# Kernel tuning notes

Hardware: AMD Instinct MI355X
Metric: run time of the kernel (lower is better)

## Reference

```python
import jax, jax.numpy as jnp
import numpy as np
import math

WS = 7          # window size (hardcoded in RelativeSinusoidalEmbeddings)
NUM_HEADS = 12

def _rel_embeddings(ws=WS):
    # Faithful replica of RelativeSinusoidalEmbeddings.__init__
    C = 2 * ws - 1
    B = np.zeros((C, C), dtype=np.float32)
    positions = np.arange(C, dtype=np.float32)[:, None]
    divisor = np.exp(np.arange(0, C, 2, dtype=np.float32) * (-math.log(10000.0) / C))
    angles = positions * divisor
    B[:, 0::2] = np.sin(angles)
    B[:, 1::2] = np.cos(angles[:, :-1])
    x = np.arange(1.0, ws + 1.0, 1.0 / ws)                 # length ws*ws
    xi = (x[None, :] - x[:, None]).astype(np.int32)        # trunc toward zero, like torch .int()
    y = np.concatenate([np.arange(1, ws + 1)] * ws)
    yi = y[None, :] - y[:, None]
    return jnp.asarray(B[xi, yi])                           # [ws^2, ws^2]

def _shift_masks(ws=WS):
    n = ws * ws
    s = ws * (ws // 2)
    row = np.zeros((n, n), dtype=np.float32)
    row[-s:, : n - s] = -np.inf
    row[: n - s, -s:] = -np.inf
    # rearrange '(r w1) (c w2) -> (w1 r) (w2 c)'
    col = row.reshape(ws, ws, ws, ws).transpose(1, 0, 3, 2).reshape(n, n)
    return jnp.asarray(row), jnp.asarray(col)

_EMB = _rel_embeddings()
_ROW_MASK, _COL_MASK = _shift_masks()

def setup_inputs() -> dict:
    key = jax.random.key(0)
    k1, k2, k3 = jax.random.split(key, 3)
    B, H, W, D = 16, 56, 56, 384
    return {
        "x": jax.random.normal(k1, (B, H, W, D), dtype=jnp.float32),
        "w_qkv": jax.random.normal(k2, (D, 3 * D), dtype=jnp.float32) * 0.02,
        "b_qkv": jnp.zeros((3 * D,), dtype=jnp.float32),
        "w_out": jax.random.normal(k3, (D, D), dtype=jnp.float32) * 0.02,
        "b_out": jnp.zeros((D,), dtype=jnp.float32),
    }

def reference(x, w_qkv, b_qkv, w_out, b_out):
    B, Hh, Ww, d = x.shape
    ws, nh = WS, NUM_HEADS
    E = d // nh
    h, w = Hh // ws, Ww // ws
    # qkv projection, split last dim as (c, K=3) per rearrange 'b h w (c K)'
    qkv = (x @ w_qkv + b_qkv).reshape(B, Hh, Ww, d, 3)
    # mask is active since Hh != 7; shift is -ws//2 == -4 (faithful to source)
    qkv = jnp.roll(qkv, (-ws // 2, -ws // 2), axis=(1, 2))
    # 'b (h m1) (w m2) (H E) K -> b H h w (m1 m2) E K'
    qkv = qkv.reshape(B, h, ws, w, ws, nh, E, 3)
    qkv = qkv.transpose(0, 5, 1, 3, 2, 4, 6, 7).reshape(B, nh, h, w, ws * ws, E, 3)
    Q, K, V = qkv[..., 0], qkv[..., 1], qkv[..., 2]
    scores = jnp.einsum('bnhwqe,bnhwke->bnhwqk', Q, K) / math.sqrt(d / nh)
    scores = scores + _EMB
    scores = scores.at[:, :, -1, :].add(_ROW_MASK)   # last row of window grid
    scores = scores.at[:, :, :, -1].add(_COL_MASK)   # last col of window grid
    att = jax.nn.softmax(scores, axis=-1) @ V         # [B, nh, h, w, ws^2, E]
    # 'b H h w (m1 m2) E -> b (h m1) (w m2) (H E)'
    out = att.reshape(B, nh, h, w, ws, ws, E)
    out = out.transpose(0, 2, 4, 3, 5, 1, 6).reshape(B, Hh, Ww, d)
    out = jnp.roll(out, (ws // 2, ws // 2), axis=(1, 2))  # unshift by +3 (as in source)
    return out @ w_out + b_out
```

## Files before the change

### kernel.cpp

```cpp
#include <hip/hip_runtime.h>
#include <math.h>

#define DIM   384
#define NQKV  1152
#define IMG   56
#define ROWS_PER_B (IMG*IMG)

typedef unsigned short u16;
typedef unsigned int u32;
typedef __attribute__((ext_vector_type(2))) unsigned int u32x2;
typedef __attribute__((ext_vector_type(4))) float f32x4;
typedef __attribute__((ext_vector_type(8))) short s16x8;

__device__ __forceinline__ u16 f2b(float f) {
    unsigned u = __float_as_uint(f);
    return (u16)((u + 0x7fffu + ((u >> 16) & 1u)) >> 16);
}

__device__ __forceinline__ void gl2lds16(const void* g, void* l) {
    __builtin_amdgcn_global_load_lds(
        (const __attribute__((address_space(1))) void*)g,
        (__attribute__((address_space(3))) void*)l, 16, 0, 0);
}

__global__ __launch_bounds__(256) void emb4_init_kernel(float* __restrict__ emb4) {
    int idx = blockIdx.x * 256 + threadIdx.x;
    if (idx >= 64 * 64) return;
    int q = idx >> 6, k = idx & 63;

    bool pad = (q >= 49) || (k >= 49);
    float base = 0.f;
    if (!pad) {
        const double step  = 1.0 / 7.0;
        const double delta = __dsub_rn(__dadd_rn(1.0, step), 1.0);
        double xk = __dadd_rn(1.0, __dmul_rn((double)k, delta));
        double xq = __dadd_rn(1.0, __dmul_rn((double)q, delta));
        int xi = (int)__dsub_rn(xk, xq);
        int yi = (k % 7) - (q % 7);
        int r = xi % 13; if (r < 0) r += 13;
        int c = yi % 13; if (c < 0) c += 13;
        const float scl = (float)(-0.7084877209212449);
        if ((c & 1) == 0) base = sinf((float)r * expf((float)c * scl));
        else              base = cosf((float)r * expf((float)(c - 1) * scl));
    }
    bool rmask = !pad && ((q >= 28) != (k >= 28));
    bool cmask = !pad && ((q % 7 >= 4) != (k % 7 >= 4));
    #pragma unroll
    for (int v = 0; v < 4; ++v) {
        float val = base;
        if (pad || ((v & 1) && rmask) || ((v & 2) && cmask)) val = -INFINITY;
        emb4[v * 4096 + idx] = val;
    }
}

__global__ __launch_bounds__(256) void cvt_f32_bf16(
    const float* __restrict__ in, u16* __restrict__ out, int n4) {
    int i = blockIdx.x * 256 + threadIdx.x;
    if (i >= n4) return;
    float4 v = ((const float4*)in)[i];
    ushort4 o;
    o.x = f2b(v.x); o.y = f2b(v.y); o.z = f2b(v.z); o.w = f2b(v.w);
    ((ushort4*)out)[i] = o;
}

__global__ __launch_bounds__(256) void cvt_transpose_bf16(
    const float* __restrict__ w, u16* __restrict__ wt, int R, int C) {
    int i = blockIdx.x * 256 + threadIdx.x;
    if (i >= R * C) return;
    int r = i / C, c = i % C;
    wt[(size_t)c * R + r] = f2b(w[i]);
}

__global__ __launch_bounds__(256) void cvt_transpose_qkv(
    const float* __restrict__ w, u16* __restrict__ wt) {
    int i = blockIdx.x * 256 + threadIdx.x;
    if (i >= 384 * 1152) return;
    int k = i / 1152, col = i % 1152;
    int ch = col / 3, comp = col % 3;
    int np = comp * 384 + ch;
    wt[(size_t)np * 384 + k] = f2b(w[i]);
}

__global__ __launch_bounds__(256) void bias_perm_kernel(
    const float* __restrict__ b, float* __restrict__ bp) {
    int n = blockIdx.x * 256 + threadIdx.x;
    if (n >= 1152) return;
    int comp = n / 384, ch = n % 384;
    bp[n] = b[ch * 3 + comp];
}

template <int MODE>
__global__ __launch_bounds__(512, 6) void mfma_gemm(
    const u16* __restrict__ A, const u16* __restrict__ Bt,
    const float* __restrict__ bias,
    u16* __restrict__ outb, float* __restrict__ outf,
    int N, int K)
{
    __shared__ __align__(16) u16 As[2][8192];
    __shared__ __align__(16) u16 Bs[8192];

    const int tid  = threadIdx.x;
    const int lane = tid & 63;
    const int wid  = tid >> 6;
    const int wr   = wid >> 2, wc = wid & 3;
    const int l15  = lane & 15, l4 = lane >> 4;

    const int gx  = gridDim.x;
    const int nwg = gx * gridDim.y;
    int wg  = blockIdx.y * gx + blockIdx.x;
    int q8  = nwg >> 3, r8 = nwg & 7;
    int xcd = wg & 7, idx = wg >> 3;
    int nid = (xcd < r8 ? xcd * (q8 + 1) : r8 * (q8 + 1) + (xcd - r8) * q8) + idx;
    const int bm = nid / gx, bn = nid % gx;

    const int srow  = lane >> 3;
    const int sslot = (lane & 7) ^ srow;
    const u16* pA[2];
    const u16* pB[2];
    #pragma unroll
    for (int i = 0; i < 2; ++i) {
        pA[i] = A  + (size_t)(bm * 128 + wid * 16 + i * 8 + srow) * K + sslot * 8;
        pB[i] = Bt + (size_t)(bn * 128 + wid * 16 + i * 8 + srow) * K + sslot * 8;
    }

    f32x4 acc[4][2] = {};
    const int NT = K >> 6;

    #define STAGE_A(t, b)                                                     \
        do {                                                                  \
            const int _kt = (t) << 6;                                         \
            _Pragma("unroll")                                                 \
            for (int _i = 0; _i < 2; ++_i)                                    \
                gl2lds16(pA[_i] + _kt, &As[b][(wid * 16 + _i * 8) * 64]);     \
        } while (0)
    #define STAGE_B(t)                                                        \
        do {                                                                  \
            const int _kt = (t) << 6;                                         \
            _Pragma("unroll")                                                 \
            for (int _i = 0; _i < 2; ++_i)                                    \
                gl2lds16(pB[_i] + _kt, &Bs[(wid * 16 + _i * 8) * 64]);        \
        } while (0)

    STAGE_A(0, 0);
    STAGE_B(0);

    for (int t = 0; t < NT; ++t) {
        const int buf = t & 1;
        if (t + 1 < NT) {
            STAGE_A(t + 1, buf ^ 1);
            asm volatile("s_waitcnt vmcnt(2)" ::: "memory");
        } else {
            asm volatile("s_waitcnt vmcnt(0)" ::: "memory");
        }
        __builtin_amdgcn_s_barrier();
        __builtin_amdgcn_sched_barrier(0);

        #pragma unroll
        for (int kk = 0; kk < 2; ++kk) {
            s16x8 af[4], bf[2];
            #pragma unroll
            for (int m = 0; m < 4; ++m) {
                int rm = wr * 64 + m * 16 + l15;
                int sl = (kk * 4 + l4) ^ (rm & 7);
                af[m] = *(const s16x8*)&As[buf][rm * 64 + sl * 8];
            }
            #pragma unroll
            for (int n = 0; n < 2; ++n) {
                int rn = wc * 32 + n * 16 + l15;
                int sl = (kk * 4 + l4) ^ (rn & 7);
                bf[n] = *(const s16x8*)&Bs[rn * 64 + sl * 8];
            }
            #pragma unroll
            for (int m = 0; m < 4; ++m)
                #pragma unroll
                for (int n = 0; n < 2; ++n)
                    acc[m][n] = __builtin_amdgcn_mfma_f32_16x16x32_bf16(
                        af[m], bf[n], acc[m][n], 0, 0, 0);
        }

        if (t + 1 < NT) {
            asm volatile("s_waitcnt lgkmcnt(0)" ::: "memory");
            __builtin_amdgcn_sched_barrier(0);
            __builtin_amdgcn_s_barrier();
            STAGE_B(t + 1);
        }
    }
    #undef STAGE_A
    #undef STAGE_B

    const int grow0 = bm * 128 + wr * 64;
    const int gcol0 = bn * 128 + wc * 32;
    #pragma unroll
    for (int m = 0; m < 4; ++m) {
        #pragma unroll
        for (int n = 0; n < 2; ++n) {
            int col = gcol0 + n * 16 + l15;
            float bz = bias[col];
            #pragma unroll
            for (int r = 0; r < 4; ++r) {
                int row = grow0 + m * 16 + l4 * 4 + r;
                float v = acc[m][n][r] + bz;
                if constexpr (MODE == 0)
                    outb[(size_t)row * N + col] = f2b(v);
                else
                    outf[(size_t)row * N + col] = v;
            }
        }
    }
}

__global__ __launch_bounds__(256) void attn_mfma_kernel(
    const u16* __restrict__ qkv, const float* __restrict__ emb4,
    u16* __restrict__ att)
{
    __shared__ __align__(16) u16 P4[4][64 * 72];
    __shared__ int rowIn[64];
    __shared__ int rowOut[64];

    const int tid  = threadIdx.x;
    const int lane = tid & 63;
    const int wid  = tid >> 6;
    const int l15  = lane & 15, l4 = lane >> 4;

    const int blk = blockIdx.x;
    const int hg  = blk % 3;
    const int win = (blk / 3) & 63;
    const int b   = blk / 192;
    const int bw  = win & 7, bh = win >> 3;
    const int head = hg * 4 + wid;

    if (tid < 64) {
        int pix = tid;
        int gr = (bh * 7 + pix / 7 + 4) % IMG;
        int gc = (bw * 7 + pix % 7 + 4) % IMG;
        rowIn[pix] = (b * IMG + gr) * IMG + gc;
    } else if (tid < 128) {
        int q = tid - 64;
        int fr = (bh * 7 + q / 7 + 3) % IMG;
        int fc = (bw * 7 + q % 7 + 3) % IMG;
        rowOut[q] = (b * IMG + fr) * IMG + fc;
    }
    __syncthreads();

    s16x8 qf[4], kf[4];
    #pragma unroll
    for (int n = 0; n < 4; ++n) {
        int pix = n * 16 + l15;
        size_t base = (size_t)rowIn[pix] * NQKV + head * 32 + l4 * 8;
        qf[n] = *(const s16x8*)(qkv + base);
        kf[n] = *(const s16x8*)(qkv + base + 384);
    }
    s16x8 vf[2][2];
    #pragma unroll
    for (int kh = 0; kh < 2; ++kh)
        #pragma unroll
        for (int ne = 0; ne < 2; ++ne)
            #pragma unroll
            for (int j = 0; j < 8; ++j) {
                int pix = kh * 32 + l4 * 8 + j;
                vf[kh][ne][j] = (short)qkv[(size_t)rowIn[pix] * NQKV + 768
                                           + head * 32 + ne * 16 + l15];
            }

    const float* ev = emb4 + ((bh == 7 ? 1 : 0) + (bw == 7 ? 2 : 0)) * 4096;

    float4 ecur[4], enxt[4];
    #pragma unroll
    for (int m = 0; m < 4; ++m)
        ecur[m] = *(const float4*)(ev + (size_t)l15 * 64 + m * 16 + l4 * 4);

    f32x4 sc[4][4] = {};
    __builtin_amdgcn_s_setprio(1);
    #pragma unroll
    for (int m = 0; m < 4; ++m)
        #pragma unroll
        for (int n = 0; n < 4; ++n)
            sc[m][n] = __builtin_amdgcn_mfma_f32_16x16x32_bf16(
                kf[m], qf[n], sc[m][n], 0, 0, 0);
    __builtin_amdgcn_s_setprio(0);

    const float scale = 0.17677669529663687f;
    u16* P = P4[wid];
    u32* P32 = (u32*)P;

    #pragma unroll
    for (int n = 0; n < 4; ++n) {
        if (n < 3) {
            #pragma unroll
            for (int m = 0; m < 4; ++m)
                enxt[m] = *(const float4*)(ev + (size_t)((n + 1) * 16 + l15) * 64
                                           + m * 16 + l4 * 4);
        }
        const int q = n * 16 + l15;
        float vals[4][4];
        float mx = -INFINITY;
        #pragma unroll
        for (int m = 0; m < 4; ++m) {
            #pragma unroll
            for (int r = 0; r < 4; ++r) {
                float v = sc[m][n][r] * scale + ((const float*)&ecur[m])[r];
                vals[m][r] = v;
                mx = fmaxf(mx, v);
            }
        }
        mx = fmaxf(mx, __shfl_xor(mx, 16));
        mx = fmaxf(mx, __shfl_xor(mx, 32));
        float sum = 0.f;
        #pragma unroll
        for (int m = 0; m < 4; ++m)
            #pragma unroll
            for (int r = 0; r < 4; ++r) {
                float p = __expf(vals[m][r] - mx);
                vals[m][r] = p;
                sum += p;
            }
        sum += __shfl_xor(sum, 16);
        sum += __shfl_xor(sum, 32);
        float inv = 1.f / sum;
        #pragma unroll
        for (int m = 0; m < 4; ++m) {
            u32x2 w;
            w[0] = (u32)f2b(vals[m][0] * inv) | ((u32)f2b(vals[m][1] * inv) << 16);
            w[1] = (u32)f2b(vals[m][2] * inv) | ((u32)f2b(vals[m][3] * inv) << 16);
            int bidx = q * 36 + m * 8 + l4 * 2;
            *(u32x2*)&P32[bidx] = w;
        }
        #pragma unroll
        for (int m = 0; m < 4; ++m) ecur[m] = enxt[m];
    }

    f32x4 o[4][2] = {};
    #pragma unroll
    for (int kh = 0; kh < 2; ++kh) {
        s16x8 pf[4];
        #pragma unroll
        for (int mq = 0; mq < 4; ++mq)
            pf[mq] = *(const s16x8*)&P[(mq * 16 + l15) * 72 + kh * 32 + l4 * 8];
        __builtin_amdgcn_s_setprio(1);
        #pragma unroll
        for (int mq = 0; mq < 4; ++mq)
            #pragma unroll
            for (int ne = 0; ne < 2; ++ne)
                o[mq][ne] = __builtin_amdgcn_mfma_f32_16x16x32_bf16(
                    pf[mq], vf[kh][ne], o[mq][ne], 0, 0, 0);
        __builtin_amdgcn_s_setprio(0);
    }

    #pragma unroll
    for (int mq = 0; mq < 4; ++mq) {
        #pragma unroll
        for (int r = 0; r < 4; ++r) {
            int q = mq * 16 + l4 * 4 + r;
            if (q < 49) {
                size_t rowb = (size_t)rowOut[q] * DIM + head * 32;
                #pragma unroll
                for (int ne = 0; ne < 2; ++ne)
                    att[rowb + ne * 16 + l15] = f2b(o[mq][ne][r]);
            }
        }
    }
}

extern "C" void kernel_launch(void* const* d_in, const int* in_sizes, int n_in,
                              void* d_out, int out_size, void* d_ws, size_t ws_size,
                              hipStream_t stream) {
    const float* x     = (const float*)d_in[0];
    const float* w_qkv = (const float*)d_in[1];
    const float* b_qkv = (const float*)d_in[2];
    const float* w_out = (const float*)d_in[3];
    const float* b_out = (const float*)d_in[4];
    float* out = (float*)d_out;

    char* wsp = (char*)d_ws;
    float* emb4  = (float*)wsp;
    u16*   wqkvt = (u16*)(wsp + 65536);
    u16*   woutt = (u16*)(wsp + 65536 + 884736);
    float* bqkvp = (float*)(wsp + 65536 + 884736 + 294912);
    const size_t fixed = 65536 + 884736 + 294912 + 4608;

    const size_t perb = (size_t)ROWS_PER_B * (DIM + NQKV + DIM) * 2;
    int nb = 16;
    while (nb > 2 && fixed + (size_t)nb * perb > ws_size) nb >>= 1;

    u16* xb   = (u16*)(wsp + fixed);
    u16* qkvb = xb   + (size_t)nb * ROWS_PER_B * DIM;
    u16* attb = qkvb + (size_t)nb * ROWS_PER_B * NQKV;

    emb4_init_kernel<<<16, 256, 0, stream>>>(emb4);
    cvt_transpose_qkv<<<(384 * 1152 + 255) / 256, 256, 0, stream>>>(w_qkv, wqkvt);
    cvt_transpose_bf16<<<(384 * 384 + 255) / 256, 256, 0, stream>>>(w_out, woutt, 384, 384);
    bias_perm_kernel<<<5, 256, 0, stream>>>(b_qkv, bqkvp);

    for (int b0 = 0; b0 < 16; b0 += nb) {
        const int rows = nb * ROWS_PER_B;
        const float* xa = x + (size_t)b0 * ROWS_PER_B * DIM;

        cvt_f32_bf16<<<(rows * DIM / 4 + 255) / 256, 256, 0, stream>>>(
            xa, xb, rows * DIM / 4);

        mfma_gemm<0><<<dim3(NQKV / 128, rows / 128), 512, 0, stream>>>(
            xb, wqkvt, bqkvp, qkvb, nullptr, NQKV, DIM);

        attn_mfma_kernel<<<nb * 192, 256, 0, stream>>>(qkvb, emb4, attb);

        mfma_gemm<1><<<dim3(DIM / 128, rows / 128), 512, 0, stream>>>(
            attb, woutt, b_out, nullptr, out + (size_t)b0 * ROWS_PER_B * DIM, DIM, DIM);
    }
}
```

Before: 163.3 us.

## Fuse fp32-to-bf16 input conversion into QKV GEMM A-operand loads

Removes the separate kernel that converted x to bf16. The QKV GEMM now reads fp32 x directly from global memory into registers and packs it to bf16 per MFMA fragment, while only the weight tile is staged through a double-buffered LDS pipeline. This drops a full write and re-read of the bf16 copy of x and frees workspace. In exchange, each column-tile block re-reads fp32 A (twice the bytes) with unstaged, latency-exposed global loads inside the k-loop.

```diff
diff --git a/kernel.cpp b/kernel.cpp
--- a/kernel.cpp
+++ b/kernel.cpp
@@ -21,6 +21,15 @@
     __builtin_amdgcn_global_load_lds(
         (const __attribute__((address_space(1))) void*)g,
         (__attribute__((address_space(3))) void*)l, 16, 0, 0);
+}
+
+__device__ __forceinline__ s16x8 pack8(float4 a, float4 b) {
+    s16x8 w;
+    w[0] = (short)f2b(a.x); w[1] = (short)f2b(a.y);
+    w[2] = (short)f2b(a.z); w[3] = (short)f2b(a.w);
+    w[4] = (short)f2b(b.x); w[5] = (short)f2b(b.y);
+    w[6] = (short)f2b(b.z); w[7] = (short)f2b(b.w);
+    return w;
 }
 
 __global__ __launch_bounds__(256) void emb4_init_kernel(float* __restrict__ emb4) {
@@ -53,16 +62,6 @@
     }
 }
 
-__global__ __launch_bounds__(256) void cvt_f32_bf16(
-    const float* __restrict__ in, u16* __restrict__ out, int n4) {
-    int i = blockIdx.x * 256 + threadIdx.x;
-    if (i >= n4) return;
-    float4 v = ((const float4*)in)[i];
-    ushort4 o;
-    o.x = f2b(v.x); o.y = f2b(v.y); o.z = f2b(v.z); o.w = f2b(v.w);
-    ((ushort4*)out)[i] = o;
-}
-
 __global__ __launch_bounds__(256) void cvt_transpose_bf16(
     const float* __restrict__ w, u16* __restrict__ wt, int R, int C) {
     int i = blockIdx.x * 256 + threadIdx.x;
@@ -89,11 +88,117 @@
     bp[n] = b[ch * 3 + comp];
 }
 
-template <int MODE>
-__global__ __launch_bounds__(512, 6) void mfma_gemm(
+__global__ __launch_bounds__(512, 6) void mfma_gemm_qkv(
+    const float* __restrict__ X, const u16* __restrict__ Bt,
+    const float* __restrict__ bias, u16* __restrict__ outb,
+    int N, int K)
+{
+    __shared__ __align__(16) u16 Bs[2][8192];
+
+    const int tid  = threadIdx.x;
+    const int lane = tid & 63;
+    const int wid  = tid >> 6;
+    const int wr   = wid >> 2, wc = wid & 3;
+    const int l15  = lane & 15, l4 = lane >> 4;
+
+    const int gx  = gridDim.x;
+    const int nwg = gx * gridDim.y;
+    int wg  = blockIdx.y * gx + blockIdx.x;
+    int q8  = nwg >> 3, r8 = nwg & 7;
+    int xcd = wg & 7, idx = wg >> 3;
+    int nid = (xcd < r8 ? xcd * (q8 + 1) : r8 * (q8 + 1) + (xcd - r8) * q8) + idx;
+    const int bm = nid / gx, bn = nid % gx;
+
+    const int srow  = lane >> 3;
+    const int sslot = (lane & 7) ^ srow;
+    const u16* pB[2];
+    #pragma unroll
+    for (int i = 0; i < 2; ++i)
+        pB[i] = Bt + (size_t)(bn * 128 + wid * 16 + i * 8 + srow) * K + sslot * 8;
+
+    const float* xrow[4];
+    #pragma unroll
+    for (int m = 0; m < 4; ++m)
+        xrow[m] = X + (size_t)(bm * 128 + wr * 64 + m * 16 + l15) * K + l4 * 8;
+
+    f32x4 acc[4][2] = {};
+    const int NT = K >> 6;
+
+    #define STAGE_B(t, b)                                                     \
+        do {                                                                  \
+            const int _kt = (t) << 6;                                         \
+            _Pragma("unroll")                                                 \
+            for (int _i = 0; _i < 2; ++_i)                                    \
+                gl2lds16(pB[_i] + _kt, &Bs[b][(wid * 16 + _i * 8) * 64]);     \
+        } while (0)
+
+    STAGE_B(0, 0);
+    STAGE_B(1, 1);
+
+    for (int t = 0; t < NT; ++t) {
+        const int buf = t & 1;
+        if (t + 1 < NT) {
+            asm volatile("s_waitcnt vmcnt(2)" ::: "memory");
+        } else {
+            asm volatile("s_waitcnt vmcnt(0)" ::: "memory");
+        }
+        __builtin_amdgcn_s_barrier();
+        __builtin_amdgcn_sched_barrier(0);
+
+        const int kt = t << 6;
+        #pragma unroll
+        for (int kk = 0; kk < 2; ++kk) {
+            s16x8 af[4], bf[2];
+            #pragma unroll
+            for (int m = 0; m < 4; ++m) {
+                const float* p = xrow[m] + kt + kk * 32;
+                float4 lo = *(const float4*)(p);
+                float4 hi = *(const float4*)(p + 4);
+                af[m] = pack8(lo, hi);
+            }
+            #pragma unroll
+            for (int n = 0; n < 2; ++n) {
+                int rn = wc * 32 + n * 16 + l15;
+                int sl = (kk * 4 + l4) ^ (rn & 7);
+                bf[n] = *(const s16x8*)&Bs[buf][rn * 64 + sl * 8];
+            }
+            #pragma unroll
+            for (int m = 0; m < 4; ++m)
+                #pragma unroll
+                for (int n = 0; n < 2; ++n)
+                    acc[m][n] = __builtin_amdgcn_mfma_f32_16x16x32_bf16(
+                        af[m], bf[n], acc[m][n], 0, 0, 0);
+        }
+
+        if (t + 2 < NT) {
+            asm volatile("s_waitcnt lgkmcnt(0)" ::: "memory");
+            __builtin_amdgcn_sched_barrier(0);
+            __builtin_amdgcn_s_barrier();
+            STAGE_B(t + 2, buf);
+        }
+    }
+    #undef STAGE_B
+
+    const int grow0 = bm * 128 + wr * 64;
+    const int gcol0 = bn * 128 + wc * 32;
+    #pragma unroll
+    for (int m = 0; m < 4; ++m) {
+        #pragma unroll
+        for (int n = 0; n < 2; ++n) {
+            int col = gcol0 + n * 16 + l15;
+            float bz = bias[col];
+            #pragma unroll
+            for (int r = 0; r < 4; ++r) {
+                int row = grow0 + m * 16 + l4 * 4 + r;
+                outb[(size_t)row * N + col] = f2b(acc[m][n][r] + bz);
+            }
+        }
+    }
+}
+
+__global__ __launch_bounds__(512, 6) void mfma_gemm_out(
     const u16* __restrict__ A, const u16* __restrict__ Bt,
-    const float* __restrict__ bias,
-    u16* __restrict__ outb, float* __restrict__ outf,
+    const float* __restrict__ bias, float* __restrict__ outf,
     int N, int K)
 {
     __shared__ __align__(16) u16 As[2][8192];
@@ -199,11 +304,7 @@
             #pragma unroll
             for (int r = 0; r < 4; ++r) {
                 int row = grow0 + m * 16 + l4 * 4 + r;
-                float v = acc[m][n][r] + bz;
-                if constexpr (MODE == 0)
-                    outb[(size_t)row * N + col] = f2b(v);
-                else
-                    outf[(size_t)row * N + col] = v;
+                outf[(size_t)row * N + col] = acc[m][n][r] + bz;
             }
         }
     }
@@ -378,12 +479,11 @@
     float* bqkvp = (float*)(wsp + 65536 + 884736 + 294912);
     const size_t fixed = 65536 + 884736 + 294912 + 4608;
 
-    const size_t perb = (size_t)ROWS_PER_B * (DIM + NQKV + DIM) * 2;
+    const size_t perb = (size_t)ROWS_PER_B * (NQKV + DIM) * 2;
     int nb = 16;
     while (nb > 2 && fixed + (size_t)nb * perb > ws_size) nb >>= 1;
 
-    u16* xb   = (u16*)(wsp + fixed);
-    u16* qkvb = xb   + (size_t)nb * ROWS_PER_B * DIM;
+    u16* qkvb = (u16*)(wsp + fixed);
     u16* attb = qkvb + (size_t)nb * ROWS_PER_B * NQKV;
 
     emb4_init_kernel<<<16, 256, 0, stream>>>(emb4);
@@ -395,15 +495,12 @@
         const int rows = nb * ROWS_PER_B;
         const float* xa = x + (size_t)b0 * ROWS_PER_B * DIM;
 
-        cvt_f32_bf16<<<(rows * DIM / 4 + 255) / 256, 256, 0, stream>>>(
-            xa, xb, rows * DIM / 4);
-
-        mfma_gemm<0><<<dim3(NQKV / 128, rows / 128), 512, 0, stream>>>(
-            xb, wqkvt, bqkvp, qkvb, nullptr, NQKV, DIM);
+        mfma_gemm_qkv<<<dim3(NQKV / 128, rows / 128), 512, 0, stream>>>(
+            xa, wqkvt, bqkvp, qkvb, NQKV, DIM);
 
         attn_mfma_kernel<<<nb * 192, 256, 0, stream>>>(qkvb, emb4, attb);
 
-        mfma_gemm<1><<<dim3(DIM / 128, rows / 128), 512, 0, stream>>>(
-            attb, woutt, b_out, nullptr, out + (size_t)b0 * ROWS_PER_B * DIM, DIM, DIM);
-    }
-}
+        mfma_gemm_out<<<dim3(DIM / 128, rows / 128), 512, 0, stream>>>(
+            attb, woutt, b_out, out + (size_t)b0 * ROWS_PER_B * DIM, DIM, DIM);
+    }
+}
```

Measured after the change: 486.6 us. 198% more time.
